# Kernel optimization log

Hardware: AMD Instinct MI355X
Metric: run time of the kernel (lower is better)

## Reference

```python
import jax, jax.numpy as jnp
import numpy as np

NEG_INF = -1e20  # the repo defines INF = 1e20
TOPK = 10


def setup_inputs() -> dict:
    key = jax.random.key(0)
    k1, k2 = jax.random.split(key)
    B, N, D, H = 8, 2048, 512, 512
    context = jax.random.normal(k1, (B, N, D), dtype=jnp.float32)
    ctx_mask = jnp.ones((B, N), dtype=jnp.int32)  # all positions valid
    W = jax.random.normal(k2, (H, D), dtype=jnp.float32) * 0.02  # linear_sim weight
    return {"context": context, "W": W, "ctx_mask": ctx_mask}


def reference(context, W, ctx_mask):
    # context_fc = relu(linear_sim(context))        : [B, N, H]
    ctx_fc = jax.nn.relu(jnp.einsum('bnd,hd->bnh', context, W))
    # attention = context_fc @ context_fc^T         : [B, N, N]
    att = jnp.einsum('bnh,bmh->bnm', ctx_fc, ctx_fc)
    # masked_fill where ctx_mask == 0 (both row and column)
    m = ctx_mask.astype(bool)
    att = jnp.where(m[:, None, :], att, NEG_INF)
    att = jnp.where(m[:, :, None], att, NEG_INF)
    # build_knn_neighbourhood: keep top-k per row, everything else -INF
    k = min(TOPK, att.shape[-1])
    knn_val, knn_ind = jax.lax.top_k(att, k)  # [B, N, k]
    B, N, _ = att.shape
    bi = jnp.arange(B)[:, None, None]
    ri = jnp.arange(N)[None, :, None]
    adj = jnp.full(att.shape, NEG_INF, dtype=att.dtype).at[bi, ri, knn_ind].set(knn_val)
    return adj
```

## Files before the change

kernel.cpp:

```cpp
#include <hip/hip_runtime.h>
#include <hip/hip_bf16.h>

#define NEG_INF -1e20f

typedef __bf16 bf16x8 __attribute__((ext_vector_type(8)));
typedef float  f32x4  __attribute__((ext_vector_type(4)));

__device__ inline unsigned short f2bf(float x) {
    unsigned u = __float_as_uint(x);
    unsigned r = u + 0x7fffu + ((u >> 16) & 1u);
    return (unsigned short)(r >> 16);
}
__device__ inline float bf2f(unsigned short h) {
    return __uint_as_float((unsigned)h << 16);
}
__device__ inline unsigned fkey(float f) {
    unsigned u = __float_as_uint(f);
    return (u & 0x80000000u) ? ~u : (u | 0x80000000u);
}
__device__ inline float unfkey(unsigned k) {
    unsigned fu = (k & 0x80000000u) ? (k ^ 0x80000000u) : ~k;
    return __uint_as_float(fu);
}

__global__ __launch_bounds__(256) void split3_all(
        const float* __restrict__ ctx, const float* __restrict__ W,
        unsigned short* __restrict__ C1, unsigned short* __restrict__ C2,
        unsigned short* __restrict__ C3, unsigned short* __restrict__ W1,
        unsigned short* __restrict__ W2, unsigned short* __restrict__ W3) {
    const int b = blockIdx.x;
    const int t = threadIdx.x;
    const float* src;
    unsigned short *p1, *p2, *p3;
    int base;
    if (b < 2048) { src = ctx; p1 = C1; p2 = C2; p3 = C3; base = b * 1024; }
    else          { src = W;   p1 = W1; p2 = W2; p3 = W3; base = (b - 2048) * 1024; }
#pragma unroll
    for (int it = 0; it < 4; ++it) {
        int i = base + it * 256 + t;
        float4 v = ((const float4*)src)[i];
        ushort4 a, bb, c;
        float r;
        a.x = f2bf(v.x); r = v.x - bf2f(a.x); bb.x = f2bf(r); c.x = f2bf(r - bf2f(bb.x));
        a.y = f2bf(v.y); r = v.y - bf2f(a.y); bb.y = f2bf(r); c.y = f2bf(r - bf2f(bb.y));
        a.z = f2bf(v.z); r = v.z - bf2f(a.z); bb.z = f2bf(r); c.z = f2bf(r - bf2f(bb.z));
        a.w = f2bf(v.w); r = v.w - bf2f(a.w); bb.w = f2bf(r); c.w = f2bf(r - bf2f(bb.w));
        ((ushort4*)p1)[i] = a;
        ((ushort4*)p2)[i] = bb;
        ((ushort4*)p3)[i] = c;
    }
}

__global__ __launch_bounds__(256, 2) void fc_mfma6(
        const unsigned short* __restrict__ A1, const unsigned short* __restrict__ A2,
        const unsigned short* __restrict__ A3, const unsigned short* __restrict__ B1,
        const unsigned short* __restrict__ B2, const unsigned short* __restrict__ B3,
        unsigned short* __restrict__ Fhi, unsigned short* __restrict__ Flo) {
    __shared__ char lds[49152];

    const int t     = threadIdx.x;
    const int mBase = blockIdx.x * 128;
    const int hBase = blockIdx.y * 128;
    const int w = t >> 6, lane = t & 63;
    const int q = lane >> 4, ln = lane & 15;
    const int wn = (w >> 1) * 64;
    const int wm = (w & 1) * 64;

    f32x4 acc[4][4] = {};

    for (int kt = 0; kt < 512; kt += 32) {
#pragma unroll
        for (int p = 0; p < 3; ++p) {
            const unsigned short* pl = (p == 0) ? A1 : (p == 1) ? A2 : A3;
#pragma unroll
            for (int rr = 0; rr < 2; ++rr) {
                int chunk = rr * 256 + t;
                int row   = chunk >> 2;
                int c     = (chunk & 3) ^ ((row >> 1) & 3);
                const unsigned short* g = pl + ((size_t)(mBase + row) * 512 + kt + c * 8);
                char* l = lds + p * 8192 + chunk * 16;
                __builtin_amdgcn_global_load_lds(
                    (const __attribute__((address_space(1))) void*)g,
                    (__attribute__((address_space(3))) void*)l, 16, 0, 0);
            }
        }
#pragma unroll
        for (int p = 0; p < 3; ++p) {
            const unsigned short* pl = (p == 0) ? B1 : (p == 1) ? B2 : B3;
#pragma unroll
            for (int rr = 0; rr < 2; ++rr) {
                int chunk = rr * 256 + t;
                int row   = chunk >> 2;
                int c     = (chunk & 3) ^ ((row >> 1) & 3);
                const unsigned short* g = pl + ((size_t)(hBase + row) * 512 + kt + c * 8);
                char* l = lds + 24576 + p * 8192 + chunk * 16;
                __builtin_amdgcn_global_load_lds(
                    (const __attribute__((address_space(1))) void*)g,
                    (__attribute__((address_space(3))) void*)l, 16, 0, 0);
            }
        }
        __syncthreads();

        bf16x8 a1[4], a2[4], a3[4], b1[4], b2[4], b3[4];
#pragma unroll
        for (int i = 0; i < 4; ++i) {
            int mA = wn + i * 16 + ln;
            int oA = (mA * 4 + (q ^ ((mA >> 1) & 3))) * 16;
            a1[i] = *(const bf16x8*)(lds +     0 + oA);
            a2[i] = *(const bf16x8*)(lds +  8192 + oA);
            a3[i] = *(const bf16x8*)(lds + 16384 + oA);
            int mB = wm + i * 16 + ln;
            int oB = (mB * 4 + (q ^ ((mB >> 1) & 3))) * 16;
            b1[i] = *(const bf16x8*)(lds + 24576 + oB);
            b2[i] = *(const bf16x8*)(lds + 32768 + oB);
            b3[i] = *(const bf16x8*)(lds + 40960 + oB);
        }
#pragma unroll
        for (int i = 0; i < 4; ++i)
#pragma unroll
            for (int j = 0; j < 4; ++j) {
                acc[i][j] = __builtin_amdgcn_mfma_f32_16x16x32_bf16(a1[i], b1[j], acc[i][j], 0, 0, 0);
                acc[i][j] = __builtin_amdgcn_mfma_f32_16x16x32_bf16(a1[i], b2[j], acc[i][j], 0, 0, 0);
                acc[i][j] = __builtin_amdgcn_mfma_f32_16x16x32_bf16(a2[i], b1[j], acc[i][j], 0, 0, 0);
                acc[i][j] = __builtin_amdgcn_mfma_f32_16x16x32_bf16(a2[i], b2[j], acc[i][j], 0, 0, 0);
                acc[i][j] = __builtin_amdgcn_mfma_f32_16x16x32_bf16(a1[i], b3[j], acc[i][j], 0, 0, 0);
                acc[i][j] = __builtin_amdgcn_mfma_f32_16x16x32_bf16(a3[i], b1[j], acc[i][j], 0, 0, 0);
            }
        __syncthreads();
    }

    unsigned* tb = (unsigned*)(lds + w * 4352);
    const int rg = lane >> 4;
    const int c4 = lane & 15;
#pragma unroll
    for (int i = 0; i < 4; ++i) {
#pragma unroll
        for (int j = 0; j < 4; ++j)
#pragma unroll
            for (int r = 0; r < 4; ++r) {
                float v = fmaxf(acc[i][j][r], 0.f);
                unsigned short hi = f2bf(v);
                unsigned short lo = f2bf(v - bf2f(hi));
                tb[(q * 4 + r) * 68 + j * 16 + ln] =
                    (unsigned)hi | ((unsigned)lo << 16);
            }
#pragma unroll
        for (int it = 0; it < 4; ++it) {
            int row = it * 4 + rg;
            uint4 pk = *(const uint4*)&tb[row * 68 + c4 * 4];
            ushort4 h, l;
            h.x = (unsigned short)pk.x; l.x = (unsigned short)(pk.x >> 16);
            h.y = (unsigned short)pk.y; l.y = (unsigned short)(pk.y >> 16);
            h.z = (unsigned short)pk.z; l.z = (unsigned short)(pk.z >> 16);
            h.w = (unsigned short)pk.w; l.w = (unsigned short)(pk.w >> 16);
            size_t off = (size_t)(mBase + wn + i * 16 + row) * 512 + hBase + wm + c4 * 4;
            *(ushort4*)(Fhi + off) = h;
            *(ushort4*)(Flo + off) = l;
        }
    }
}

__device__ __forceinline__ void select10(const float* prow, int g,
        unsigned& c0k, int& c0c, unsigned& c1k, int& c1c) {
    unsigned k[16];
#pragma unroll
    for (int s = 0; s < 4; ++s) {
        float4 v = *(const float4*)(prow + s * 4);
        k[s*4+0] = fkey(v.x); k[s*4+1] = fkey(v.y);
        k[s*4+2] = fkey(v.z); k[s*4+3] = fkey(v.w);
    }
    unsigned h1 = k[0]; int i1 = 0;
#pragma unroll
    for (int j = 1; j < 16; ++j) if (k[j] > h1) { h1 = k[j]; i1 = j; }
    unsigned h2 = 0; int i2 = 0;
#pragma unroll
    for (int j = 0; j < 16; ++j) { bool ok = (j != i1) && (k[j] > h2); h2 = ok ? k[j] : h2; i2 = ok ? j : i2; }
    bool h2v = true; unsigned taken = 0;
    c0k = 0; c0c = 0; c1k = 0; c1c = 0;
#pragma unroll
    for (int r = 0; r < 10; ++r) {
        unsigned long long P = ((unsigned long long)h1 << 32) | (unsigned)(g * 16 + i1);
#pragma unroll
        for (int off = 1; off < 8; off <<= 1) {
            unsigned long long Q = __shfl_xor(P, off, 64);
            P = (Q > P) ? Q : P;
        }
        unsigned M = (unsigned)(P >> 32);
        int cl = (int)(P & 0xffffu);
        if (r < 8) { if (g == r)     { c0k = M; c0c = cl; } }
        else       { if (g == r - 8) { c1k = M; c1c = cl; } }
        if ((cl >> 4) == g) {
            taken |= 1u << (cl & 15);
            if (h2v) { h1 = h2; i1 = i2; h2v = false; }
            else {
                unsigned bh = 0; int bi = 0;
#pragma unroll
                for (int jx = 0; jx < 16; ++jx) {
                    bool ok = (((taken >> jx) & 1u) == 0u) && (k[jx] > bh);
                    bh = ok ? k[jx] : bh; bi = ok ? jx : bi;
                }
                h1 = bh; i1 = bi;
            }
        }
    }
}

__global__ __launch_bounds__(256, 2) void att_cand(
        const unsigned short* __restrict__ Fhi, const unsigned short* __restrict__ Flo,
        const int* __restrict__ mask, float* __restrict__ cvO,
        unsigned short* __restrict__ ciO) {
    __shared__ char lds[32768];

    const int t = threadIdx.x;
    const int b = blockIdx.x & 7;
    int p = blockIdx.x >> 3, ti = 0;
    while (p >= 16 - ti) { p -= 16 - ti; ++ti; }
    const int tj = ti + p;
    const int nBase = ti * 128;
    const int mBase = tj * 128;
    const int w    = t >> 6, lane = t & 63;
    const int q    = lane >> 4, ln = lane & 15;
    const int wn   = (w >> 1) * 64;
    const int wm   = (w & 1) * 64;
    const size_t rowB = (size_t)b * 2048;

    f32x4 acc[4][4] = {};

    for (int kt = 0; kt < 512; kt += 32) {
#pragma unroll
        for (int pp = 0; pp < 4; ++pp) {
            const unsigned short* plane = (pp & 1) ? Flo : Fhi;
            int rbase = (pp < 2) ? nBase : mBase;
#pragma unroll
            for (int r = 0; r < 2; ++r) {
                int chunk = r * 256 + t;
                int row   = chunk >> 2;
                int c     = (chunk & 3) ^ ((row >> 1) & 3);
                const unsigned short* g =
                    plane + ((rowB + rbase + row) * 512 + kt + c * 8);
                char* l = lds + pp * 8192 + chunk * 16;
                __builtin_amdgcn_global_load_lds(
                    (const __attribute__((address_space(1))) void*)g,
                    (__attribute__((address_space(3))) void*)l, 16, 0, 0);
            }
        }
        __syncthreads();

        bf16x8 ah[4], al[4], bh[4], bl[4];
#pragma unroll
        for (int i = 0; i < 4; ++i) {
            int mA = wn + i * 16 + ln;
            int oA = (mA * 4 + (q ^ ((mA >> 1) & 3))) * 16;
            ah[i] = *(const bf16x8*)(lds +     0 + oA);
            al[i] = *(const bf16x8*)(lds +  8192 + oA);
            int mB = wm + i * 16 + ln;
            int oB = (mB * 4 + (q ^ ((mB >> 1) & 3))) * 16;
            bh[i] = *(const bf16x8*)(lds + 16384 + oB);
            bl[i] = *(const bf16x8*)(lds + 24576 + oB);
        }
#pragma unroll
        for (int i = 0; i < 4; ++i)
#pragma unroll
            for (int j = 0; j < 4; ++j) {
                acc[i][j] = __builtin_amdgcn_mfma_f32_16x16x32_bf16(ah[i], bh[j], acc[i][j], 0, 0, 0);
                acc[i][j] = __builtin_amdgcn_mfma_f32_16x16x32_bf16(ah[i], bl[j], acc[i][j], 0, 0, 0);
                acc[i][j] = __builtin_amdgcn_mfma_f32_16x16x32_bf16(al[i], bh[j], acc[i][j], 0, 0, 0);
            }
        __syncthreads();
    }

    float* patch = (float*)lds;
    const int* mb = mask + b * 2048;

    int cmj[4];
#pragma unroll
    for (int j = 0; j < 4; ++j) cmj[j] = mb[mBase + wm + j * 16 + ln];
    int rmAll[4][4];
#pragma unroll
    for (int i = 0; i < 4; ++i)
#pragma unroll
        for (int r = 0; r < 4; ++r) rmAll[i][r] = mb[nBase + wn + i * 16 + q * 4 + r];

    const int pr = t >> 3, g = t & 7;

#pragma unroll
    for (int i = 0; i < 4; ++i) {
        int prBase = (w >> 1) * 16;
#pragma unroll
        for (int j = 0; j < 4; ++j)
#pragma unroll
            for (int r = 0; r < 4; ++r) {
                float v = ((rmAll[i][r] != 0) & (cmj[j] != 0)) ? acc[i][j][r] : NEG_INF;
                patch[(prBase + q * 4 + r) * 132 + wm + j * 16 + ln] = v;
            }
        __syncthreads();
        {
            unsigned c0k, c1k; int c0c, c1c;
            select10(patch + pr * 132 + g * 16, g, c0k, c0c, c1k, c1c);
            int rowG = nBase + ((pr >> 4) << 6) + i * 16 + (pr & 15);
            size_t cb = (((size_t)b * 2048 + rowG) * 16 + tj) * 10;
            cvO[cb + g] = unfkey(c0k);
            ciO[cb + g] = (unsigned short)(mBase + c0c);
            if (g < 2) {
                cvO[cb + 8 + g] = unfkey(c1k);
                ciO[cb + 8 + g] = (unsigned short)(nBase == mBase ? mBase + c1c : mBase + c1c);
            }
        }
        __syncthreads();
    }

    if (ti != tj) {
#pragma unroll
        for (int c2 = 0; c2 < 4; ++c2) {
            if ((w & 1) == (c2 >> 1)) {
                int jb = (c2 & 1) * 2;
#pragma unroll
                for (int jj = 0; jj < 2; ++jj) {
                    int j = jb + jj;
#pragma unroll
                    for (int i2 = 0; i2 < 4; ++i2)
#pragma unroll
                        for (int r = 0; r < 4; ++r) {
                            float v = ((rmAll[i2][r] != 0) & (cmj[j] != 0)) ? acc[i2][j][r] : NEG_INF;
                            patch[(jj * 16 + ln) * 132 + wn + i2 * 16 + q * 4 + r] = v;
                        }
                }
            }
            __syncthreads();
            {
                unsigned c0k, c1k; int c0c, c1c;
                select10(patch + pr * 132 + g * 16, g, c0k, c0c, c1k, c1c);
                int rowG = mBase + c2 * 32 + pr;
                size_t cb = (((size_t)b * 2048 + rowG) * 16 + ti) * 10;
                cvO[cb + g] = unfkey(c0k);
                ciO[cb + g] = (unsigned short)(nBase + c0c);
                if (g < 2) {
                    cvO[cb + 8 + g] = unfkey(c1k);
                    ciO[cb + 8 + g] = (unsigned short)(nBase + c1c);
                }
            }
            __syncthreads();
        }
    }
}

__global__ __launch_bounds__(256) void topk_merge(
        const float* __restrict__ cv, const unsigned short* __restrict__ ci,
        float* __restrict__ out) {
    __shared__ float patch[4][2048];

    const int t = threadIdx.x, w = t >> 6, lane = t & 63;
    const size_t R = (size_t)blockIdx.x * 4 + w;
    const float* v = cv + R * 160;
    const unsigned short* id = ci + R * 160;

    float v0 = v[lane], v1 = v[lane + 64];
    int   c0 = id[lane], c1 = id[lane + 64];
    float v2 = NEG_INF;  int c2 = 0;
    if (lane < 32) { v2 = v[lane + 128]; c2 = id[lane + 128]; }
    unsigned k0 = fkey(v0), k1 = fkey(v1), k2 = fkey(v2);

    unsigned h1 = k0; int i1 = 0;
    if (k1 > h1) { h1 = k1; i1 = 1; }
    if (k2 > h1) { h1 = k2; i1 = 2; }
    unsigned taken = 0;
    unsigned myk = 0; int mycol = 0;

    for (int r = 0; r < 10; ++r) {
        unsigned M = h1;
#pragma unroll
        for (int off = 1; off < 64; off <<= 1) {
            unsigned o = __shfl_xor(M, off, 64);
            M = (o > M) ? o : M;
        }
        unsigned long long ball = __ballot(h1 == M);
        int src = __ffsll(ball) - 1;
        int csel = (i1 == 0) ? c0 : ((i1 == 1) ? c1 : c2);
        int wcol = __shfl(csel, src, 64);
        if (lane == r) { myk = M; mycol = wcol; }
        if (lane == src) {
            taken |= 1u << i1;
            unsigned bh = 0; int bi = 0;
            if (!(taken & 1u))            { bh = k0; bi = 0; }
            if (!(taken & 2u) && k1 > bh) { bh = k1; bi = 1; }
            if (!(taken & 4u) && k2 > bh) { bh = k2; bi = 2; }
            h1 = bh; i1 = bi;
        }
    }

    float* pw = patch[w];
    float4 ninf4 = make_float4(NEG_INF, NEG_INF, NEG_INF, NEG_INF);
#pragma unroll
    for (int s = 0; s < 8; ++s) ((float4*)pw)[s * 64 + lane] = ninf4;
    if (lane < 10) pw[mycol] = unfkey(myk);
    float* row = out + R * 2048;
#pragma unroll
    for (int s = 0; s < 8; ++s)
        ((float4*)row)[s * 64 + lane] = ((float4*)pw)[s * 64 + lane];
}

extern "C" void kernel_launch(void* const* d_in, const int* in_sizes, int n_in,
                              void* d_out, int out_size, void* d_ws, size_t ws_size,
                              hipStream_t stream) {
    const float* ctx  = (const float*)d_in[0];
    const float* W    = (const float*)d_in[1];
    const int*   mask = (const int*)d_in[2];
    float* out = (float*)d_out;

    const size_t CN = (size_t)16384 * 512;
    const size_t WN = (size_t)512 * 512;
    unsigned short* C1 = (unsigned short*)d_out;
    unsigned short* C2 = C1 + CN;
    unsigned short* C3 = C2 + CN;
    unsigned short* W1 = C3 + CN;
    unsigned short* W2 = W1 + WN;
    unsigned short* W3 = W2 + WN;
    unsigned short* Fhi = W3 + WN;
    unsigned short* Flo = Fhi + CN;

    float* cv          = (float*)d_ws;
    unsigned short* ci = (unsigned short*)(cv + (size_t)8 * 2048 * 160);

    dim3 blk(256);
    split3_all<<<dim3(2112), blk, 0, stream>>>(ctx, W, C1, C2, C3, W1, W2, W3);
    fc_mfma6<<<dim3(128, 4), blk, 0, stream>>>(C1, C2, C3, W1, W2, W3, Fhi, Flo);
    att_cand<<<dim3(1088), blk, 0, stream>>>(Fhi, Flo, mask, cv, ci);
    topk_merge<<<dim3(4096), blk, 0, stream>>>(cv, ci, out);
}
```

Before: 356.2 us.

## Double-buffer top-k staging patch and use float ballot-based selection

Replaces the 64-bit key-packed shuffle reduction in the per-row top-10 selection with a float max reduction followed by a ballot and a lane lookup to find the winner's column. Merges the row and mirrored-column selection passes into one loop over a double-buffered LDS patch, so the next patch is staged while the current one is selected. This cuts the barriers per pass from two to one. It also raises launch bounds to 3 blocks per CU and enlarges LDS slightly, which may constrain registers and cause spills in the MFMA accumulator path.

```diff
diff --git a/kernel.cpp b/kernel.cpp
--- a/kernel.cpp
+++ b/kernel.cpp
@@ -160,44 +160,45 @@
     }
 }
 
-__device__ __forceinline__ void select10(const float* prow, int g,
-        unsigned& c0k, int& c0c, unsigned& c1k, int& c1c) {
-    unsigned k[16];
+__device__ __forceinline__ void select10f(const float* prow, int lane,
+        float& c0v, int& c0c, float& c1v, int& c1c) {
+    const int g = lane & 7;
+    float v[16];
 #pragma unroll
     for (int s = 0; s < 4; ++s) {
-        float4 v = *(const float4*)(prow + s * 4);
-        k[s*4+0] = fkey(v.x); k[s*4+1] = fkey(v.y);
-        k[s*4+2] = fkey(v.z); k[s*4+3] = fkey(v.w);
-    }
-    unsigned h1 = k[0]; int i1 = 0;
-#pragma unroll
-    for (int j = 1; j < 16; ++j) if (k[j] > h1) { h1 = k[j]; i1 = j; }
-    unsigned h2 = 0; int i2 = 0;
-#pragma unroll
-    for (int j = 0; j < 16; ++j) { bool ok = (j != i1) && (k[j] > h2); h2 = ok ? k[j] : h2; i2 = ok ? j : i2; }
+        float4 t4 = *(const float4*)(prow + s * 4);
+        v[s*4+0] = t4.x; v[s*4+1] = t4.y; v[s*4+2] = t4.z; v[s*4+3] = t4.w;
+    }
+    float h1 = v[0]; int i1 = 0;
+#pragma unroll
+    for (int j = 1; j < 16; ++j) { bool c = v[j] > h1; h1 = c ? v[j] : h1; i1 = c ? j : i1; }
+    float h2 = -3e38f; int i2 = 0;
+#pragma unroll
+    for (int j = 0; j < 16; ++j) { bool c = (j != i1) && (v[j] > h2); h2 = c ? v[j] : h2; i2 = c ? j : i2; }
     bool h2v = true; unsigned taken = 0;
-    c0k = 0; c0c = 0; c1k = 0; c1c = 0;
+    c0v = NEG_INF; c0c = 0; c1v = NEG_INF; c1c = 0;
 #pragma unroll
     for (int r = 0; r < 10; ++r) {
-        unsigned long long P = ((unsigned long long)h1 << 32) | (unsigned)(g * 16 + i1);
-#pragma unroll
-        for (int off = 1; off < 8; off <<= 1) {
-            unsigned long long Q = __shfl_xor(P, off, 64);
-            P = (Q > P) ? Q : P;
-        }
-        unsigned M = (unsigned)(P >> 32);
-        int cl = (int)(P & 0xffffu);
-        if (r < 8) { if (g == r)     { c0k = M; c0c = cl; } }
-        else       { if (g == r - 8) { c1k = M; c1c = cl; } }
-        if ((cl >> 4) == g) {
-            taken |= 1u << (cl & 15);
+        float M = h1;
+        M = fmaxf(M, __shfl_xor(M, 1, 64));
+        M = fmaxf(M, __shfl_xor(M, 2, 64));
+        M = fmaxf(M, __shfl_xor(M, 4, 64));
+        unsigned long long ball = __ballot(h1 == M);
+        int base = lane & ~7;
+        int srcg = __ffsll((unsigned long long)((ball >> base) & 0xFFull)) - 1;
+        int il   = __shfl(i1, base + srcg, 64);
+        int col  = srcg * 16 + il;
+        if (r < 8) { if (g == r)     { c0v = M; c0c = col; } }
+        else       { if (g == r - 8) { c1v = M; c1c = col; } }
+        if (g == srcg) {
+            taken |= 1u << i1;
             if (h2v) { h1 = h2; i1 = i2; h2v = false; }
             else {
-                unsigned bh = 0; int bi = 0;
+                float bh = -3e38f; int bi = 0;
 #pragma unroll
                 for (int jx = 0; jx < 16; ++jx) {
-                    bool ok = (((taken >> jx) & 1u) == 0u) && (k[jx] > bh);
-                    bh = ok ? k[jx] : bh; bi = ok ? jx : bi;
+                    bool ok = (((taken >> jx) & 1u) == 0u) && (v[jx] > bh);
+                    bh = ok ? v[jx] : bh; bi = ok ? jx : bi;
                 }
                 h1 = bh; i1 = bi;
             }
@@ -205,17 +206,17 @@
     }
 }
 
-__global__ __launch_bounds__(256, 2) void att_cand(
+__global__ __launch_bounds__(256, 3) void att_cand(
         const unsigned short* __restrict__ Fhi, const unsigned short* __restrict__ Flo,
         const int* __restrict__ mask, float* __restrict__ cvO,
         unsigned short* __restrict__ ciO) {
-    __shared__ char lds[32768];
+    __shared__ char lds[34816];
 
     const int t = threadIdx.x;
     const int b = blockIdx.x & 7;
-    int p = blockIdx.x >> 3, ti = 0;
-    while (p >= 16 - ti) { p -= 16 - ti; ++ti; }
-    const int tj = ti + p;
+    int p0 = blockIdx.x >> 3, ti = 0;
+    while (p0 >= 16 - ti) { p0 -= 16 - ti; ++ti; }
+    const int tj = ti + p0;
     const int nBase = ti * 128;
     const int mBase = tj * 128;
     const int w    = t >> 6, lane = t & 63;
@@ -282,62 +283,64 @@
         for (int r = 0; r < 4; ++r) rmAll[i][r] = mb[nBase + wn + i * 16 + q * 4 + r];
 
     const int pr = t >> 3, g = t & 7;
-
-#pragma unroll
-    for (int i = 0; i < 4; ++i) {
+    const int nPass = (ti != tj) ? 8 : 4;
+
+    auto stageRow = [&](int i, float* buf) {
         int prBase = (w >> 1) * 16;
 #pragma unroll
         for (int j = 0; j < 4; ++j)
 #pragma unroll
             for (int r = 0; r < 4; ++r) {
-                float v = ((rmAll[i][r] != 0) & (cmj[j] != 0)) ? acc[i][j][r] : NEG_INF;
-                patch[(prBase + q * 4 + r) * 132 + wm + j * 16 + ln] = v;
-            }
-        __syncthreads();
-        {
-            unsigned c0k, c1k; int c0c, c1c;
-            select10(patch + pr * 132 + g * 16, g, c0k, c0c, c1k, c1c);
-            int rowG = nBase + ((pr >> 4) << 6) + i * 16 + (pr & 15);
-            size_t cb = (((size_t)b * 2048 + rowG) * 16 + tj) * 10;
-            cvO[cb + g] = unfkey(c0k);
-            ciO[cb + g] = (unsigned short)(mBase + c0c);
+                float vv = ((rmAll[i][r] != 0) & (cmj[j] != 0)) ? acc[i][j][r] : NEG_INF;
+                buf[(prBase + q * 4 + r) * 132 + wm + j * 16 + ln] = vv;
+            }
+    };
+    auto stageMir = [&](int c2, float* buf) {
+        if ((w & 1) == (c2 >> 1)) {
+            int jb = (c2 & 1) * 2;
+#pragma unroll
+            for (int jj = 0; jj < 2; ++jj) {
+                int j = jb + jj;
+#pragma unroll
+                for (int i2 = 0; i2 < 4; ++i2)
+#pragma unroll
+                    for (int r = 0; r < 4; ++r) {
+                        float vv = ((rmAll[i2][r] != 0) & (cmj[j] != 0)) ? acc[i2][j][r] : NEG_INF;
+                        buf[(jj * 16 + ln) * 132 + wn + i2 * 16 + q * 4 + r] = vv;
+                    }
+            }
+        }
+    };
+
+    stageRow(0, patch);
+    __syncthreads();
+
+#pragma unroll
+    for (int p = 0; p < 8; ++p) {
+        if (p < nPass) {
+            if (p + 1 < nPass) {
+                float* nbuf = patch + ((p + 1) & 1) * 4224;
+                if (p + 1 < 4) stageRow(p + 1, nbuf);
+                else           stageMir(p + 1 - 4, nbuf);
+            }
+            float c0v, c1v; int c0c, c1c;
+            const float* prow = patch + (p & 1) * 4224 + pr * 132 + g * 16;
+            select10f(prow, lane, c0v, c0c, c1v, c1c);
+
+            int rowG, slot, colbase;
+            if (p < 4) {
+                rowG = nBase + ((pr >> 4) << 6) + p * 16 + (pr & 15);
+                slot = tj; colbase = mBase;
+            } else {
+                rowG = mBase + (p - 4) * 32 + pr;
+                slot = ti; colbase = nBase;
+            }
+            size_t cb = (((size_t)b * 2048 + rowG) * 16 + slot) * 10;
+            cvO[cb + g] = c0v;
+            ciO[cb + g] = (unsigned short)(colbase + c0c);
             if (g < 2) {
-                cvO[cb + 8 + g] = unfkey(c1k);
-                ciO[cb + 8 + g] = (unsigned short)(nBase == mBase ? mBase + c1c : mBase + c1c);
-            }
-        }
-        __syncthreads();
-    }
-
-    if (ti != tj) {
-#pragma unroll
-        for (int c2 = 0; c2 < 4; ++c2) {
-            if ((w & 1) == (c2 >> 1)) {
-                int jb = (c2 & 1) * 2;
-#pragma unroll
-                for (int jj = 0; jj < 2; ++jj) {
-                    int j = jb + jj;
-#pragma unroll
-                    for (int i2 = 0; i2 < 4; ++i2)
-#pragma unroll
-                        for (int r = 0; r < 4; ++r) {
-                            float v = ((rmAll[i2][r] != 0) & (cmj[j] != 0)) ? acc[i2][j][r] : NEG_INF;
-                            patch[(jj * 16 + ln) * 132 + wn + i2 * 16 + q * 4 + r] = v;
-                        }
-                }
-            }
-            __syncthreads();
-            {
-                unsigned c0k, c1k; int c0c, c1c;
-                select10(patch + pr * 132 + g * 16, g, c0k, c0c, c1k, c1c);
-                int rowG = mBase + c2 * 32 + pr;
-                size_t cb = (((size_t)b * 2048 + rowG) * 16 + ti) * 10;
-                cvO[cb + g] = unfkey(c0k);
-                ciO[cb + g] = (unsigned short)(nBase + c0c);
-                if (g < 2) {
-                    cvO[cb + 8 + g] = unfkey(c1k);
-                    ciO[cb + 8 + g] = (unsigned short)(nBase + c1c);
-                }
+                cvO[cb + 8 + g] = c1v;
+                ciO[cb + 8 + g] = (unsigned short)(colbase + c1c);
             }
             __syncthreads();
         }
```

Result: faster. 347.8 us (-2.4%).
